# Kernel tuning notes

Hardware: AMD Instinct MI355X
Metric: run time of the kernel (lower is better)

Reference implementation:

```python
import jax, jax.numpy as jnp
import numpy as np

D_MODEL = 512
N_HEADS = 8
D_HEAD = D_MODEL // N_HEADS
D_FF = 2048
LN_EPS = 1e-5


def _layer_norm(x, g, b):
    mu = jnp.mean(x, axis=-1, keepdims=True)
    var = jnp.var(x, axis=-1, keepdims=True)
    return (x - mu) * jax.lax.rsqrt(var + LN_EPS) * g + b


def setup_inputs() -> dict:
    key = jax.random.key(0)
    ks = jax.random.split(key, 16)
    s_d = 1.0 / np.sqrt(D_MODEL)
    s_f = 1.0 / np.sqrt(D_FF)
    x = jax.random.normal(ks[0], (32, 512, D_MODEL), dtype=jnp.float32)
    # per-head Q/K/V linears stacked over heads: [H, D, dh] weights, [H, dh] biases
    Wq = jax.random.uniform(ks[1], (N_HEADS, D_MODEL, D_HEAD), jnp.float32, -s_d, s_d)
    bq = jax.random.uniform(ks[2], (N_HEADS, D_HEAD), jnp.float32, -s_d, s_d)
    Wk = jax.random.uniform(ks[3], (N_HEADS, D_MODEL, D_HEAD), jnp.float32, -s_d, s_d)
    bk = jax.random.uniform(ks[4], (N_HEADS, D_HEAD), jnp.float32, -s_d, s_d)
    Wv = jax.random.uniform(ks[5], (N_HEADS, D_MODEL, D_HEAD), jnp.float32, -s_d, s_d)
    bv = jax.random.uniform(ks[6], (N_HEADS, D_HEAD), jnp.float32, -s_d, s_d)
    Wo = jax.random.uniform(ks[7], (D_MODEL, D_MODEL), jnp.float32, -s_d, s_d)
    bo = jax.random.uniform(ks[8], (D_MODEL,), jnp.float32, -s_d, s_d)
    ln1_g = jnp.ones((D_MODEL,), jnp.float32)
    ln1_b = jnp.zeros((D_MODEL,), jnp.float32)
    W1 = jax.random.uniform(ks[9], (D_MODEL, D_FF), jnp.float32, -s_d, s_d)
    b1 = jax.random.uniform(ks[10], (D_FF,), jnp.float32, -s_d, s_d)
    W2 = jax.random.uniform(ks[11], (D_FF, D_MODEL), jnp.float32, -s_f, s_f)
    b2 = jax.random.uniform(ks[12], (D_MODEL,), jnp.float32, -s_f, s_f)
    ln2_g = jnp.ones((D_MODEL,), jnp.float32)
    ln2_b = jnp.zeros((D_MODEL,), jnp.float32)
    return dict(x=x, Wq=Wq, bq=bq, Wk=Wk, bk=bk, Wv=Wv, bv=bv, Wo=Wo, bo=bo,
                ln1_g=ln1_g, ln1_b=ln1_b, W1=W1, b1=b1, W2=W2, b2=b2,
                ln2_g=ln2_g, ln2_b=ln2_b)


def reference(x, Wq, bq, Wk, bk, Wv, bv, Wo, bo, ln1_g, ln1_b, W1, b1, W2, b2, ln2_g, ln2_b):
    B, T, D = x.shape
    # batched-heads Q/K/V: [B, H, T, dh]
    q = jnp.einsum('btd,hde->bhte', x, Wq) + bq[None, :, None, :]
    k = jnp.einsum('btd,hde->bhte', x, Wk) + bk[None, :, None, :]
    v = jnp.einsum('btd,hde->bhte', x, Wv) + bv[None, :, None, :]
    scale = D_HEAD ** -0.5
    scores = jnp.einsum('bhte,bhse->bhts', q, k) * scale  # [B,H,T,T]
    causal = jnp.tril(jnp.ones((T, T), dtype=bool))
    scores = jnp.where(causal[None, None], scores, -jnp.inf)
    w = jax.nn.softmax(scores, axis=-1)
    o = jnp.einsum('bhts,bhse->bhte', w, v)              # [B,H,T,dh]
    o = jnp.transpose(o, (0, 2, 1, 3)).reshape(B, T, D)   # concat heads
    attn = o @ Wo + bo
    out1 = x + _layer_norm(attn, ln1_g, ln1_b)            # post-LN on sublayer output (as in source)
    ff = jax.nn.relu(out1 @ W1 + b1) @ W2 + b2
    return out1 + _layer_norm(ff, ln2_g, ln2_b)
```

## Files before the change

kernel.cpp:

```cpp
#include <hip/hip_runtime.h>
#include <hip/hip_bf16.h>


#define D_MODEL 512
#define N_HEADS 8
#define D_HEAD 64
#define D_FF 2048
#define NROWS 16384

typedef __bf16 bf16x8 __attribute__((ext_vector_type(8)));
typedef float f32x4 __attribute__((ext_vector_type(4)));
typedef float f32x16 __attribute__((ext_vector_type(16)));

#define SWZ(x) ((x) ^ ((((x) >> 7) & 7) << 4))

static __device__ __forceinline__ ushort f2bf(float f) {
    union { float f; unsigned u; } v; v.f = f;
    unsigned r = v.u + 0x7fffu + ((v.u >> 16) & 1u);
    return (ushort)(r >> 16);
}
static __device__ __forceinline__ unsigned pack2(float lo, float hi) {
    return (unsigned)f2bf(lo) | ((unsigned)f2bf(hi) << 16);
}
static __device__ __forceinline__ void async16(const void* g, void* l) {
    __builtin_amdgcn_global_load_lds(
        (const __attribute__((address_space(1))) void*)g,
        (__attribute__((address_space(3))) void*)l, 16, 0, 0);
}

__global__ __launch_bounds__(256) void conv_bf_kernel(
    const float* __restrict__ src, ushort* __restrict__ dst, int n8)
{
    int i = blockIdx.x * 256 + threadIdx.x;
    if (i >= n8) return;
    const float4* s = (const float4*)src;
    float4 a = s[i * 2], b = s[i * 2 + 1];
    uint4 o;
    o.x = pack2(a.x, a.y); o.y = pack2(a.z, a.w);
    o.z = pack2(b.x, b.y); o.w = pack2(b.z, b.w);
    ((uint4*)dst)[i] = o;
}

static __device__ __forceinline__ void tile_transpose_body(
    const float* __restrict__ src, int srcldc, ushort* __restrict__ dst, int Rd,
    int r0, int c0)
{
    __shared__ float t[64][65];
    int tid = threadIdx.x;
    int lr = tid >> 4, lc4 = (tid & 15) * 4;
    #pragma unroll
    for (int i = 0; i < 4; ++i) {
        float4 v = *(const float4*)&src[(size_t)(r0 + lr + i * 16) * srcldc + c0 + lc4];
        t[lr + i * 16][lc4 + 0] = v.x;
        t[lr + i * 16][lc4 + 1] = v.y;
        t[lr + i * 16][lc4 + 2] = v.z;
        t[lr + i * 16][lc4 + 3] = v.w;
    }
    __syncthreads();
    int oc = tid >> 2, orr = (tid & 3) * 16;
    uint4 u0, u1;
    u0.x = pack2(t[orr + 0][oc],  t[orr + 1][oc]);
    u0.y = pack2(t[orr + 2][oc],  t[orr + 3][oc]);
    u0.z = pack2(t[orr + 4][oc],  t[orr + 5][oc]);
    u0.w = pack2(t[orr + 6][oc],  t[orr + 7][oc]);
    u1.x = pack2(t[orr + 8][oc],  t[orr + 9][oc]);
    u1.y = pack2(t[orr + 10][oc], t[orr + 11][oc]);
    u1.z = pack2(t[orr + 12][oc], t[orr + 13][oc]);
    u1.w = pack2(t[orr + 14][oc], t[orr + 15][oc]);
    ushort* d = dst + (size_t)(c0 + oc) * Rd + r0 + orr;
    *(uint4*)&d[0] = u0;
    *(uint4*)&d[8] = u1;
}

__global__ __launch_bounds__(256) void transpose_bf_kernel(
    const float* __restrict__ src, ushort* __restrict__ dst, int R, int C)
{
    tile_transpose_body(src, C, dst, R, blockIdx.y * 64, blockIdx.x * 64);
}

__global__ __launch_bounds__(256) void qkv_pack_kernel(
    const float* __restrict__ Wq, const float* __restrict__ Wk,
    const float* __restrict__ Wv, ushort* __restrict__ WpT)
{
    int z = blockIdx.z;
    int p = z >> 3, h = z & 7;
    const float* src = ((p == 0) ? Wq : (p == 1) ? Wk : Wv) + (size_t)h * D_MODEL * D_HEAD;
    ushort* dst = WpT + (size_t)(p * D_MODEL + h * D_HEAD) * D_MODEL;
    tile_transpose_body(src, D_HEAD, dst, D_MODEL, blockIdx.y * 64, 0);
}

__global__ __launch_bounds__(256) void pack_bias_kernel(
    const float* __restrict__ bq, const float* __restrict__ bk,
    const float* __restrict__ bv, float* __restrict__ bp)
{
    int idx = blockIdx.x * 256 + threadIdx.x;
    if (idx >= 3 * D_MODEL) return;
    int p = idx / D_MODEL;
    int h = (idx % D_MODEL) / D_HEAD;
    int e = idx % D_HEAD;
    const float* bb = (p == 0) ? bq : (p == 1) ? bk : bv;
    bp[idx] = bb[h * D_HEAD + e];
}

template<int OMODE, bool RELU>
__global__ __launch_bounds__(512, 1) void gemm_bf16_kernel(
    const ushort* __restrict__ A, const ushort* __restrict__ BT,
    const float* __restrict__ bias, void* __restrict__ Cout,
    ushort* __restrict__ Qg, ushort* __restrict__ Kg, ushort* __restrict__ Vt,
    int M, int N, int K, int nbx)
{
    extern __shared__ __align__(16) char smem[];

    const int tid = threadIdx.x;
    const int wid = tid >> 6, l = tid & 63;
    const int wr = wid >> 1, wc = wid & 1;

    const int total = gridDim.x;
    const int cpx = total >> 3;
    const int flat = blockIdx.x;
    const int swz = (flat & 7) * cpx + (flat >> 3);
    const int bx = swz % nbx, by = swz / nbx;
    const int m0 = by * 256, n0 = bx * 128;

    const int srow = tid >> 3;
    const int sbyte = (tid & 7) * 16;
    const int ssw = sbyte ^ ((srow & 7) << 4);

    #define STAGE(t)                                                          \
    {                                                                         \
        const int kk_ = (t) * 64;                                             \
        char* dst_ = smem + ((t) & 1) * 49152;                                \
        _Pragma("unroll")                                                     \
        for (int i = 0; i < 4; ++i)                                           \
            async16((const char*)(A + (size_t)(m0 + i * 64 + srow) * K + kk_) \
                        + ssw,                                                \
                    dst_ + i * 8192 + tid * 16);                              \
        _Pragma("unroll")                                                     \
        for (int i = 0; i < 2; ++i)                                           \
            async16((const char*)(BT + (size_t)(n0 + i * 64 + srow) * K + kk_)\
                        + ssw,                                                \
                    dst_ + 32768 + i * 8192 + tid * 16);                      \
    }

    const int fl = l & 31, fh = l >> 5;
    const int frsw = (fl & 7) << 4;

    f32x16 acc[2][2] = {};

    STAGE(0);
    const int T = K >> 6;
    for (int t = 0; t < T; ++t) {
        __builtin_amdgcn_s_barrier();
        if (t + 1 < T) {
            STAGE(t + 1);
            asm volatile("s_waitcnt vmcnt(6)" ::: "memory");
        } else {
            asm volatile("s_waitcnt vmcnt(0)" ::: "memory");
        }
        __builtin_amdgcn_sched_barrier(0);

        const char* bufA = smem + (t & 1) * 49152;
        const char* bufB = bufA + 32768;
        #pragma unroll
        for (int ks = 0; ks < 4; ++ks) {
            const int kb = ((ks * 32 + fh * 16) ^ frsw);
            bf16x8 af[2], bfv[2];
            #pragma unroll
            for (int mi = 0; mi < 2; ++mi)
                af[mi] = *(const bf16x8*)(bufA +
                    (wr * 64 + mi * 32 + fl) * 128 + kb);
            #pragma unroll
            for (int ni = 0; ni < 2; ++ni)
                bfv[ni] = *(const bf16x8*)(bufB +
                    (wc * 64 + ni * 32 + fl) * 128 + kb);
            #pragma unroll
            for (int mi = 0; mi < 2; ++mi)
                #pragma unroll
                for (int ni = 0; ni < 2; ++ni)
                    acc[mi][ni] = __builtin_amdgcn_mfma_f32_32x32x16_bf16(
                        af[mi], bfv[ni], acc[mi][ni], 0, 0, 0);
        }
    }

    #pragma unroll
    for (int ni = 0; ni < 2; ++ni) {
        const int c = n0 + wc * 64 + ni * 32 + fl;
        const float bvv = bias ? bias[c] : 0.f;
        #pragma unroll
        for (int mi = 0; mi < 2; ++mi) {
            const int rbase = m0 + wr * 64 + mi * 32 + (fh << 2);
            float vv[16];
            #pragma unroll
            for (int reg = 0; reg < 16; ++reg) {
                float v = acc[mi][ni][reg] + bvv;
                if (RELU) v = fmaxf(v, 0.f);
                vv[reg] = v;
            }
            if (OMODE == 0) {
                #pragma unroll
                for (int reg = 0; reg < 16; ++reg) {
                    int r = rbase + (reg & 3) + ((reg >> 2) << 3);
                    ((float*)Cout)[(size_t)r * N + c] = vv[reg];
                }
            } else if (OMODE == 1) {
                #pragma unroll
                for (int reg = 0; reg < 16; ++reg) {
                    int r = rbase + (reg & 3) + ((reg >> 2) << 3);
                    ((ushort*)Cout)[(size_t)r * N + c] = f2bf(vv[reg]);
                }
            } else {
                const int p = n0 >> 9;
                const int h = (c >> 6) & 7, e = c & 63;
                #pragma unroll
                for (int q = 0; q < 4; ++q) {
                    int r0 = rbase + (q << 3);
                    int b = r0 >> 9, t0 = r0 & 511;
                    size_t bh = (size_t)(b * 8 + h);
                    if (p == 2) {
                        uint2 pk;
                        pk.x = pack2(vv[q * 4 + 0], vv[q * 4 + 1]);
                        pk.y = pack2(vv[q * 4 + 2], vv[q * 4 + 3]);
                        *(uint2*)&Vt[bh * 32768 + (size_t)e * 512 + t0] = pk;
                    } else {
                        ushort* dst = (p == 0 ? Qg : Kg) + bh * 32768 +
                                      (size_t)t0 * 64 + e;
                        dst[0]   = f2bf(vv[q * 4 + 0]);
                        dst[64]  = f2bf(vv[q * 4 + 1]);
                        dst[128] = f2bf(vv[q * 4 + 2]);
                        dst[192] = f2bf(vv[q * 4 + 3]);
                    }
                }
            }
        }
    }
    #undef STAGE
}

__global__ __launch_bounds__(256) void attn_kernel(
    const ushort* __restrict__ Qg,
    const ushort* __restrict__ Kg,
    const ushort* __restrict__ Vt,
    ushort* __restrict__ O)
{
    __shared__ __align__(16) char QP[8192];
    __shared__ __align__(16) char KB[2][8192];
    __shared__ __align__(16) char VB[2][8192];

    const int bh = blockIdx.x, qb = blockIdx.y;
    const int tid = threadIdx.x;
    const int w = tid >> 6, l = tid & 63;

    const ushort* Qb = Qg + (size_t)bh * 32768;
    const ushort* Kb = Kg + (size_t)bh * 32768;
    const ushort* Vb = Vt + (size_t)bh * 32768;

    #pragma unroll
    for (int i = 0; i < 2; ++i) {
        int Xi = i * 4096 + tid * 16;
        int row = Xi >> 7;
        int sw = SWZ(Xi) & 127;
        async16((const char*)(Qb + (size_t)(qb * 64 + row) * 64) + sw, QP + Xi);
    }
    #define STAGEKV(kt, bb)                                                     \
        { _Pragma("unroll")                                                     \
          for (int i = 0; i < 2; ++i) {                                         \
              int Xi = i * 4096 + tid * 16;                                     \
              int row = Xi >> 7;                                                \
              int sw = SWZ(Xi) & 127;                                           \
              async16((const char*)(Kb + (size_t)((kt) * 64 + row) * 64) + sw,  \
                      KB[bb] + Xi);                                             \
              async16((const char*)(Vb + (size_t)row * 512 + (kt) * 64) + sw,   \
                      VB[bb] + Xi);                                             \
          } }
    STAGEKV(0, 0);
    __syncthreads();

    bf16x8 qf[2];
    {
        int qrow = w * 16 + (l & 15);
        #pragma unroll
        for (int ks = 0; ks < 2; ++ks) {
            int X = qrow * 128 + ks * 64 + (l >> 4) * 16;
            qf[ks] = *(const bf16x8*)(QP + SWZ(X));
        }
    }

    float mrow = -INFINITY, lrow = 0.f;
    f32x4 oacc[4] = {};

    for (int kt = 0; kt <= qb; ++kt) {
        int cur = kt & 1;
        if (kt < qb) STAGEKV(kt + 1, cur ^ 1);

        f32x4 sacc[4] = {};
        #pragma unroll
        for (int ks = 0; ks < 2; ++ks) {
            #pragma unroll
            for (int mi = 0; mi < 4; ++mi) {
                int X = (mi * 16 + (l & 15)) * 128 + ks * 64 + (l >> 4) * 16;
                bf16x8 kf = *(const bf16x8*)(KB[cur] + SWZ(X));
                sacc[mi] = __builtin_amdgcn_mfma_f32_16x16x32_bf16(
                    kf, qf[ks], sacc[mi], 0, 0, 0);
            }
        }

        float sv[16];
        float tmax = -INFINITY;
        const int qrow_t = w * 16 + (l & 15);
        #pragma unroll
        for (int mi = 0; mi < 4; ++mi)
            #pragma unroll
            for (int r = 0; r < 4; ++r) {
                float s = sacc[mi][r] * 0.125f;
                if (kt == qb) {
                    int key_l = mi * 16 + (l >> 4) * 4 + r;
                    if (key_l > qrow_t) s = -INFINITY;
                }
                sv[mi * 4 + r] = s;
                tmax = fmaxf(tmax, s);
            }
        tmax = fmaxf(tmax, __shfl_xor(tmax, 16));
        tmax = fmaxf(tmax, __shfl_xor(tmax, 32));
        float mnew = fmaxf(mrow, tmax);
        float corr = __expf(mrow - mnew);
        mrow = mnew;
        float psum = 0.f;
        #pragma unroll
        for (int i = 0; i < 16; ++i) { sv[i] = __expf(sv[i] - mnew); psum += sv[i]; }
        psum += __shfl_xor(psum, 16);
        psum += __shfl_xor(psum, 32);
        lrow = lrow * corr + psum;

        #pragma unroll
        for (int mi = 0; mi < 4; ++mi) {
            uint2 pk;
            pk.x = pack2(sv[mi * 4 + 0], sv[mi * 4 + 1]);
            pk.y = pack2(sv[mi * 4 + 2], sv[mi * 4 + 3]);
            int X = qrow_t * 128 + (mi * 16 + (l >> 4) * 4) * 2;
            *(uint2*)(QP + SWZ(X)) = pk;
        }

        #pragma unroll
        for (int r = 0; r < 4; ++r) {
            float cr = __shfl(corr, (l & 48) | ((l >> 4) * 4 + r));
            #pragma unroll
            for (int n = 0; n < 4; ++n) oacc[n][r] *= cr;
        }

        #pragma unroll
        for (int ks = 0; ks < 2; ++ks) {
            int Xa = qrow_t * 128 + ks * 64 + (l >> 4) * 16;
            bf16x8 pa = *(const bf16x8*)(QP + SWZ(Xa));
            #pragma unroll
            for (int n = 0; n < 4; ++n) {
                int Xb = (n * 16 + (l & 15)) * 128 + ks * 64 + (l >> 4) * 16;
                bf16x8 vb = *(const bf16x8*)(VB[cur] + SWZ(Xb));
                oacc[n] = __builtin_amdgcn_mfma_f32_16x16x32_bf16(
                    pa, vb, oacc[n], 0, 0, 0);
            }
        }
        __syncthreads();
    }

    float linv = 1.0f / lrow;
    const int b_ = bh >> 3, h_ = bh & 7;
    #pragma unroll
    for (int r = 0; r < 4; ++r) {
        float li = __shfl(linv, (l & 48) | ((l >> 4) * 4 + r));
        int trow = qb * 64 + w * 16 + (l >> 4) * 4 + r;
        size_t obase = ((size_t)b_ * 512 + trow) * 512 + h_ * 64 + (l & 15);
        #pragma unroll
        for (int n = 0; n < 4; ++n)
            O[obase + n * 16] = f2bf(oacc[n][r] * li);
    }
}

template<bool WBF>
__global__ __launch_bounds__(256) void ln_res_kernel(
    const float* __restrict__ v, const float* __restrict__ res,
    const float* __restrict__ g, const float* __restrict__ bb,
    float* __restrict__ out, ushort* __restrict__ out_bf)
{
    int row  = blockIdx.x * 4 + (threadIdx.x >> 6);
    int lane = threadIdx.x & 63;
    const float4* vp = (const float4*)(v + (size_t)row * D_MODEL);
    float4 a = vp[lane];
    float4 c = vp[lane + 64];
    float sum = a.x + a.y + a.z + a.w + c.x + c.y + c.z + c.w;
    float sq  = a.x*a.x + a.y*a.y + a.z*a.z + a.w*a.w
              + c.x*c.x + c.y*c.y + c.z*c.z + c.w*c.w;
    #pragma unroll
    for (int o = 1; o < 64; o <<= 1) {
        sum += __shfl_xor(sum, o);
        sq  += __shfl_xor(sq, o);
    }
    float mu   = sum * (1.f / 512.f);
    float var  = sq * (1.f / 512.f) - mu * mu;
    float rstd = rsqrtf(var + 1e-5f);

    const float4* rp = (const float4*)(res + (size_t)row * D_MODEL);
    const float4* gp = (const float4*)g;
    const float4* bp = (const float4*)bb;
    float4 r0 = rp[lane], r1 = rp[lane + 64];
    float4 g0 = gp[lane], g1 = gp[lane + 64];
    float4 b0 = bp[lane], b1 = bp[lane + 64];
    float4 o0, o1;
    o0.x = r0.x + (a.x - mu) * rstd * g0.x + b0.x;
    o0.y = r0.y + (a.y - mu) * rstd * g0.y + b0.y;
    o0.z = r0.z + (a.z - mu) * rstd * g0.z + b0.z;
    o0.w = r0.w + (a.w - mu) * rstd * g0.w + b0.w;
    o1.x = r1.x + (c.x - mu) * rstd * g1.x + b1.x;
    o1.y = r1.y + (c.y - mu) * rstd * g1.y + b1.y;
    o1.z = r1.z + (c.z - mu) * rstd * g1.z + b1.z;
    o1.w = r1.w + (c.w - mu) * rstd * g1.w + b1.w;
    float4* op = (float4*)(out + (size_t)row * D_MODEL);
    op[lane] = o0;
    op[lane + 64] = o1;
    if (WBF) {
        uint2 p0, p1;
        p0.x = pack2(o0.x, o0.y); p0.y = pack2(o0.z, o0.w);
        p1.x = pack2(o1.x, o1.y); p1.y = pack2(o1.z, o1.w);
        *(uint2*)&out_bf[(size_t)row * D_MODEL + lane * 4] = p0;
        *(uint2*)&out_bf[(size_t)row * D_MODEL + 256 + lane * 4] = p1;
    }
}

extern "C" void kernel_launch(void* const* d_in, const int* in_sizes, int n_in,
                              void* d_out, int out_size, void* d_ws, size_t ws_size,
                              hipStream_t stream)
{
    const float* x     = (const float*)d_in[0];
    const float* Wq    = (const float*)d_in[1];
    const float* bq    = (const float*)d_in[2];
    const float* Wk    = (const float*)d_in[3];
    const float* bk    = (const float*)d_in[4];
    const float* Wv    = (const float*)d_in[5];
    const float* bv    = (const float*)d_in[6];
    const float* Wo    = (const float*)d_in[7];
    const float* bo    = (const float*)d_in[8];
    const float* ln1_g = (const float*)d_in[9];
    const float* ln1_b = (const float*)d_in[10];
    const float* W1    = (const float*)d_in[11];
    const float* b1    = (const float*)d_in[12];
    const float* W2    = (const float*)d_in[13];
    const float* b2    = (const float*)d_in[14];
    const float* ln2_g = (const float*)d_in[15];
    const float* ln2_b = (const float*)d_in[16];

    float* ws = (float*)d_ws;
    ushort* Qg      = (ushort*)(ws);
    ushort* Kg      = (ushort*)(ws + 4194304);
    ushort* Vt      = (ushort*)(ws + 8388608);
    ushort* O_bf    = (ushort*)(ws + 12582912);
    float*  attnb   = ws + 16777216;
    float*  out1    = ws + 25165824;
    ushort* out1_bf = (ushort*)(ws + 33554432);
    ushort* x_bf    = (ushort*)(ws + 37748736);
    ushort* WpT     = (ushort*)(ws + 41943040);
    ushort* WoT     = (ushort*)(ws + 42336256);
    ushort* W1T     = (ushort*)(ws + 42467328);
    ushort* W2T     = (ushort*)(ws + 42991616);
    float*  bp      = ws + 43515904;
    ushort* ff1_bf  = (ushort*)ws;
    float*  ff2     = attnb;

    (void)hipFuncSetAttribute(
        reinterpret_cast<const void*>(&gemm_bf16_kernel<2, false>),
        hipFuncAttributeMaxDynamicSharedMemorySize, 98304);
    (void)hipFuncSetAttribute(
        reinterpret_cast<const void*>(&gemm_bf16_kernel<0, false>),
        hipFuncAttributeMaxDynamicSharedMemorySize, 98304);
    (void)hipFuncSetAttribute(
        reinterpret_cast<const void*>(&gemm_bf16_kernel<1, true>),
        hipFuncAttributeMaxDynamicSharedMemorySize, 98304);

    conv_bf_kernel<<<dim3(4096), 256, 0, stream>>>(x, x_bf, NROWS * D_MODEL / 8);
    qkv_pack_kernel<<<dim3(1, 8, 24), 256, 0, stream>>>(Wq, Wk, Wv, WpT);
    transpose_bf_kernel<<<dim3(8, 8), 256, 0, stream>>>(Wo, WoT, 512, 512);
    transpose_bf_kernel<<<dim3(32, 8), 256, 0, stream>>>(W1, W1T, 512, 2048);
    transpose_bf_kernel<<<dim3(8, 32), 256, 0, stream>>>(W2, W2T, 2048, 512);
    pack_bias_kernel<<<dim3(6), 256, 0, stream>>>(bq, bk, bv, bp);

    gemm_bf16_kernel<2, false><<<dim3(768), 512, 98304, stream>>>(
        x_bf, WpT, bp, nullptr, Qg, Kg, Vt, NROWS, 1536, 512, 12);

    attn_kernel<<<dim3(256, 8), 256, 0, stream>>>(Qg, Kg, Vt, O_bf);

    gemm_bf16_kernel<0, false><<<dim3(256), 512, 98304, stream>>>(
        O_bf, WoT, bo, attnb, nullptr, nullptr, nullptr, NROWS, 512, 512, 4);

    ln_res_kernel<true><<<dim3(NROWS / 4), 256, 0, stream>>>(
        attnb, x, ln1_g, ln1_b, out1, out1_bf);

    gemm_bf16_kernel<1, true><<<dim3(1024), 512, 98304, stream>>>(
        out1_bf, W1T, b1, ff1_bf, nullptr, nullptr, nullptr, NROWS, 2048, 512, 16);

    gemm_bf16_kernel<0, false><<<dim3(256), 512, 98304, stream>>>(
        ff1_bf, W2T, b2, ff2, nullptr, nullptr, nullptr, NROWS, 512, 2048, 4);

    ln_res_kernel<false><<<dim3(NROWS / 4), 256, 0, stream>>>(
        ff2, out1, ln2_g, ln2_b, (float*)d_out, nullptr);
}
```

Before: 224.0 us.

## Merge prep kernels, emit bf16 GEMM outputs for LN, restructure pipeline barriers

Six preprocessing launches (x conversion, weight transposes, bias pack) become a single prep kernel, cutting launch overhead. The Wo and W2 GEMMs now write bf16 instead of fp32, and the layer-norm kernels read bf16, halving that intermediate traffic. The GEMM main loop now issues the next stage's loads before computing and waits for all loads plus a barrier afterwards, in place of a partial vmcnt wait. Rounding the pre-LayerNorm activations to bf16 lowers accuracy.

```diff
diff --git a/kernel.cpp b/kernel.cpp
--- a/kernel.cpp
+++ b/kernel.cpp
@@ -22,23 +22,14 @@
 static __device__ __forceinline__ unsigned pack2(float lo, float hi) {
     return (unsigned)f2bf(lo) | ((unsigned)f2bf(hi) << 16);
 }
+static __device__ __forceinline__ float bf2f(ushort u) {
+    union { unsigned u; float f; } v; v.u = (unsigned)u << 16;
+    return v.f;
+}
 static __device__ __forceinline__ void async16(const void* g, void* l) {
     __builtin_amdgcn_global_load_lds(
         (const __attribute__((address_space(1))) void*)g,
         (__attribute__((address_space(3))) void*)l, 16, 0, 0);
-}
-
-__global__ __launch_bounds__(256) void conv_bf_kernel(
-    const float* __restrict__ src, ushort* __restrict__ dst, int n8)
-{
-    int i = blockIdx.x * 256 + threadIdx.x;
-    if (i >= n8) return;
-    const float4* s = (const float4*)src;
-    float4 a = s[i * 2], b = s[i * 2 + 1];
-    uint4 o;
-    o.x = pack2(a.x, a.y); o.y = pack2(a.z, a.w);
-    o.z = pack2(b.x, b.y); o.w = pack2(b.z, b.w);
-    ((uint4*)dst)[i] = o;
 }
 
 static __device__ __forceinline__ void tile_transpose_body(
@@ -72,34 +63,53 @@
     *(uint4*)&d[8] = u1;
 }
 
-__global__ __launch_bounds__(256) void transpose_bf_kernel(
-    const float* __restrict__ src, ushort* __restrict__ dst, int R, int C)
-{
-    tile_transpose_body(src, C, dst, R, blockIdx.y * 64, blockIdx.x * 64);
-}
-
-__global__ __launch_bounds__(256) void qkv_pack_kernel(
+__global__ __launch_bounds__(256) void prep_kernel(
+    const float* __restrict__ x, ushort* __restrict__ x_bf,
     const float* __restrict__ Wq, const float* __restrict__ Wk,
-    const float* __restrict__ Wv, ushort* __restrict__ WpT)
-{
-    int z = blockIdx.z;
-    int p = z >> 3, h = z & 7;
-    const float* src = ((p == 0) ? Wq : (p == 1) ? Wk : Wv) + (size_t)h * D_MODEL * D_HEAD;
-    ushort* dst = WpT + (size_t)(p * D_MODEL + h * D_HEAD) * D_MODEL;
-    tile_transpose_body(src, D_HEAD, dst, D_MODEL, blockIdx.y * 64, 0);
-}
-
-__global__ __launch_bounds__(256) void pack_bias_kernel(
+    const float* __restrict__ Wv, ushort* __restrict__ WpT,
+    const float* __restrict__ Wo, ushort* __restrict__ WoT,
+    const float* __restrict__ W1, ushort* __restrict__ W1T,
+    const float* __restrict__ W2, ushort* __restrict__ W2T,
     const float* __restrict__ bq, const float* __restrict__ bk,
     const float* __restrict__ bv, float* __restrict__ bp)
 {
-    int idx = blockIdx.x * 256 + threadIdx.x;
-    if (idx >= 3 * D_MODEL) return;
-    int p = idx / D_MODEL;
-    int h = (idx % D_MODEL) / D_HEAD;
-    int e = idx % D_HEAD;
-    const float* bb = (p == 0) ? bq : (p == 1) ? bk : bv;
-    bp[idx] = bb[h * D_HEAD + e];
+    const int blk = blockIdx.x;
+    const int tid = threadIdx.x;
+    if (blk < 4096) {
+        int i = blk * 256 + tid;
+        const float4* s = (const float4*)x;
+        float4 a = s[i * 2], b = s[i * 2 + 1];
+        uint4 o;
+        o.x = pack2(a.x, a.y); o.y = pack2(a.z, a.w);
+        o.z = pack2(b.x, b.y); o.w = pack2(b.z, b.w);
+        ((uint4*)x_bf)[i] = o;
+    } else if (blk < 4288) {
+        int idx = blk - 4096;
+        int z = idx >> 3, y = idx & 7;
+        int p = z >> 3, h = z & 7;
+        const float* src = ((p == 0) ? Wq : (p == 1) ? Wk : Wv) +
+                           (size_t)h * D_MODEL * D_HEAD;
+        ushort* dst = WpT + (size_t)(p * D_MODEL + h * D_HEAD) * D_MODEL;
+        tile_transpose_body(src, D_HEAD, dst, D_MODEL, y * 64, 0);
+    } else if (blk < 4352) {
+        int idx = blk - 4288;
+        tile_transpose_body(Wo, 512, WoT, 512, (idx >> 3) * 64, (idx & 7) * 64);
+    } else if (blk < 4608) {
+        int idx = blk - 4352;
+        tile_transpose_body(W1, 2048, W1T, 512, (idx >> 5) * 64, (idx & 31) * 64);
+    } else if (blk < 4864) {
+        int idx = blk - 4608;
+        tile_transpose_body(W2, 512, W2T, 2048, (idx >> 3) * 64, (idx & 7) * 64);
+    } else {
+        int gid = (blk - 4864) * 256 + tid;
+        if (gid < 3 * D_MODEL) {
+            int p = gid / D_MODEL;
+            int h = (gid % D_MODEL) / D_HEAD;
+            int e = gid % D_HEAD;
+            const float* bb = (p == 0) ? bq : (p == 1) ? bk : bv;
+            bp[gid] = bb[h * D_HEAD + e];
+        }
+    }
 }
 
 template<int OMODE, bool RELU>
@@ -115,8 +125,7 @@
     const int wid = tid >> 6, l = tid & 63;
     const int wr = wid >> 1, wc = wid & 1;
 
-    const int total = gridDim.x;
-    const int cpx = total >> 3;
+    const int cpx = gridDim.x >> 3;
     const int flat = blockIdx.x;
     const int swz = (flat & 7) * cpx + (flat >> 3);
     const int bx = swz % nbx, by = swz / nbx;
@@ -147,17 +156,14 @@
 
     f32x16 acc[2][2] = {};
 
+    const int T = K >> 6;
     STAGE(0);
-    const int T = K >> 6;
+    asm volatile("s_waitcnt vmcnt(0)" ::: "memory");
+    __builtin_amdgcn_s_barrier();
+    __builtin_amdgcn_sched_barrier(0);
+
     for (int t = 0; t < T; ++t) {
-        __builtin_amdgcn_s_barrier();
-        if (t + 1 < T) {
-            STAGE(t + 1);
-            asm volatile("s_waitcnt vmcnt(6)" ::: "memory");
-        } else {
-            asm volatile("s_waitcnt vmcnt(0)" ::: "memory");
-        }
-        __builtin_amdgcn_sched_barrier(0);
+        if (t + 1 < T) STAGE(t + 1);
 
         const char* bufA = smem + (t & 1) * 49152;
         const char* bufB = bufA + 32768;
@@ -180,7 +186,14 @@
                     acc[mi][ni] = __builtin_amdgcn_mfma_f32_32x32x16_bf16(
                         af[mi], bfv[ni], acc[mi][ni], 0, 0, 0);
         }
-    }
+
+        if (t + 1 < T) {
+            asm volatile("s_waitcnt vmcnt(0)" ::: "memory");
+            __builtin_amdgcn_s_barrier();
+            __builtin_amdgcn_sched_barrier(0);
+        }
+    }
+    #undef STAGE
 
     #pragma unroll
     for (int ni = 0; ni < 2; ++ni) {
@@ -196,13 +209,7 @@
                 if (RELU) v = fmaxf(v, 0.f);
                 vv[reg] = v;
             }
-            if (OMODE == 0) {
-                #pragma unroll
-                for (int reg = 0; reg < 16; ++reg) {
-                    int r = rbase + (reg & 3) + ((reg >> 2) << 3);
-                    ((float*)Cout)[(size_t)r * N + c] = vv[reg];
-                }
-            } else if (OMODE == 1) {
+            if (OMODE == 1) {
                 #pragma unroll
                 for (int reg = 0; reg < 16; ++reg) {
                     int r = rbase + (reg & 3) + ((reg >> 2) << 3);
@@ -233,7 +240,6 @@
             }
         }
     }
-    #undef STAGE
 }
 
 __global__ __launch_bounds__(256) void attn_kernel(
@@ -377,18 +383,24 @@
 
 template<bool WBF>
 __global__ __launch_bounds__(256) void ln_res_kernel(
-    const float* __restrict__ v, const float* __restrict__ res,
+    const ushort* __restrict__ v, const float* __restrict__ res,
     const float* __restrict__ g, const float* __restrict__ bb,
     float* __restrict__ out, ushort* __restrict__ out_bf)
 {
     int row  = blockIdx.x * 4 + (threadIdx.x >> 6);
     int lane = threadIdx.x & 63;
-    const float4* vp = (const float4*)(v + (size_t)row * D_MODEL);
-    float4 a = vp[lane];
-    float4 c = vp[lane + 64];
-    float sum = a.x + a.y + a.z + a.w + c.x + c.y + c.z + c.w;
-    float sq  = a.x*a.x + a.y*a.y + a.z*a.z + a.w*a.w
-              + c.x*c.x + c.y*c.y + c.z*c.z + c.w*c.w;
+    const int c0 = lane * 8;
+
+    uint4 vb = *(const uint4*)&v[(size_t)row * D_MODEL + c0];
+    float f[8];
+    f[0] = bf2f((ushort)(vb.x & 0xffff)); f[1] = bf2f((ushort)(vb.x >> 16));
+    f[2] = bf2f((ushort)(vb.y & 0xffff)); f[3] = bf2f((ushort)(vb.y >> 16));
+    f[4] = bf2f((ushort)(vb.z & 0xffff)); f[5] = bf2f((ushort)(vb.z >> 16));
+    f[6] = bf2f((ushort)(vb.w & 0xffff)); f[7] = bf2f((ushort)(vb.w >> 16));
+
+    float sum = 0.f, sq = 0.f;
+    #pragma unroll
+    for (int i = 0; i < 8; ++i) { sum += f[i]; sq += f[i] * f[i]; }
     #pragma unroll
     for (int o = 1; o < 64; o <<= 1) {
         sum += __shfl_xor(sum, o);
@@ -398,30 +410,29 @@
     float var  = sq * (1.f / 512.f) - mu * mu;
     float rstd = rsqrtf(var + 1e-5f);
 
-    const float4* rp = (const float4*)(res + (size_t)row * D_MODEL);
-    const float4* gp = (const float4*)g;
-    const float4* bp = (const float4*)bb;
-    float4 r0 = rp[lane], r1 = rp[lane + 64];
-    float4 g0 = gp[lane], g1 = gp[lane + 64];
-    float4 b0 = bp[lane], b1 = bp[lane + 64];
-    float4 o0, o1;
-    o0.x = r0.x + (a.x - mu) * rstd * g0.x + b0.x;
-    o0.y = r0.y + (a.y - mu) * rstd * g0.y + b0.y;
-    o0.z = r0.z + (a.z - mu) * rstd * g0.z + b0.z;
-    o0.w = r0.w + (a.w - mu) * rstd * g0.w + b0.w;
-    o1.x = r1.x + (c.x - mu) * rstd * g1.x + b1.x;
-    o1.y = r1.y + (c.y - mu) * rstd * g1.y + b1.y;
-    o1.z = r1.z + (c.z - mu) * rstd * g1.z + b1.z;
-    o1.w = r1.w + (c.w - mu) * rstd * g1.w + b1.w;
-    float4* op = (float4*)(out + (size_t)row * D_MODEL);
-    op[lane] = o0;
-    op[lane + 64] = o1;
+    float4 r0 = *(const float4*)&res[(size_t)row * D_MODEL + c0];
+    float4 r1 = *(const float4*)&res[(size_t)row * D_MODEL + c0 + 4];
+    float4 g0 = *(const float4*)&g[c0],  g1 = *(const float4*)&g[c0 + 4];
+    float4 b0 = *(const float4*)&bb[c0], b1 = *(const float4*)&bb[c0 + 4];
+
+    float o8[8];
+    o8[0] = r0.x + (f[0] - mu) * rstd * g0.x + b0.x;
+    o8[1] = r0.y + (f[1] - mu) * rstd * g0.y + b0.y;
+    o8[2] = r0.z + (f[2] - mu) * rstd * g0.z + b0.z;
+    o8[3] = r0.w + (f[3] - mu) * rstd * g0.w + b0.w;
+    o8[4] = r1.x + (f[4] - mu) * rstd * g1.x + b1.x;
+    o8[5] = r1.y + (f[5] - mu) * rstd * g1.y + b1.y;
+    o8[6] = r1.z + (f[6] - mu) * rstd * g1.z + b1.z;
+    o8[7] = r1.w + (f[7] - mu) * rstd * g1.w + b1.w;
+
+    float4* op = (float4*)&out[(size_t)row * D_MODEL + c0];
+    op[0] = make_float4(o8[0], o8[1], o8[2], o8[3]);
+    op[1] = make_float4(o8[4], o8[5], o8[6], o8[7]);
     if (WBF) {
-        uint2 p0, p1;
-        p0.x = pack2(o0.x, o0.y); p0.y = pack2(o0.z, o0.w);
-        p1.x = pack2(o1.x, o1.y); p1.y = pack2(o1.z, o1.w);
-        *(uint2*)&out_bf[(size_t)row * D_MODEL + lane * 4] = p0;
-        *(uint2*)&out_bf[(size_t)row * D_MODEL + 256 + lane * 4] = p1;
+        uint4 pk;
+        pk.x = pack2(o8[0], o8[1]); pk.y = pack2(o8[2], o8[3]);
+        pk.z = pack2(o8[4], o8[5]); pk.w = pack2(o8[6], o8[7]);
+        *(uint4*)&out_bf[(size_t)row * D_MODEL + c0] = pk;
     }
 }
 
@@ -452,52 +463,48 @@
     ushort* Kg      = (ushort*)(ws + 4194304);
     ushort* Vt      = (ushort*)(ws + 8388608);
     ushort* O_bf    = (ushort*)(ws + 12582912);
-    float*  attnb   = ws + 16777216;
-    float*  out1    = ws + 25165824;
-    ushort* out1_bf = (ushort*)(ws + 33554432);
-    ushort* x_bf    = (ushort*)(ws + 37748736);
+    ushort* attn_bf = (ushort*)(ws + 16777216);
+    float*  out1    = ws + 20971520;
+    ushort* out1_bf = (ushort*)(ws + 29360128);
+    ushort* x_bf    = (ushort*)(ws + 33554432);
+    ushort* ff2_bf  = (ushort*)(ws + 37748736);
     ushort* WpT     = (ushort*)(ws + 41943040);
     ushort* WoT     = (ushort*)(ws + 42336256);
     ushort* W1T     = (ushort*)(ws + 42467328);
     ushort* W2T     = (ushort*)(ws + 42991616);
     float*  bp      = ws + 43515904;
     ushort* ff1_bf  = (ushort*)ws;
-    float*  ff2     = attnb;
 
     (void)hipFuncSetAttribute(
         reinterpret_cast<const void*>(&gemm_bf16_kernel<2, false>),
         hipFuncAttributeMaxDynamicSharedMemorySize, 98304);
     (void)hipFuncSetAttribute(
-        reinterpret_cast<const void*>(&gemm_bf16_kernel<0, false>),
+        reinterpret_cast<const void*>(&gemm_bf16_kernel<1, false>),
         hipFuncAttributeMaxDynamicSharedMemorySize, 98304);
     (void)hipFuncSetAttribute(
         reinterpret_cast<const void*>(&gemm_bf16_kernel<1, true>),
         hipFuncAttributeMaxDynamicSharedMemorySize, 98304);
 
-    conv_bf_kernel<<<dim3(4096), 256, 0, stream>>>(x, x_bf, NROWS * D_MODEL / 8);
-    qkv_pack_kernel<<<dim3(1, 8, 24), 256, 0, stream>>>(Wq, Wk, Wv, WpT);
-    transpose_bf_kernel<<<dim3(8, 8), 256, 0, stream>>>(Wo, WoT, 512, 512);
-    transpose_bf_kernel<<<dim3(32, 8), 256, 0, stream>>>(W1, W1T, 512, 2048);
-    transpose_bf_kernel<<<dim3(8, 32), 256, 0, stream>>>(W2, W2T, 2048, 512);
-    pack_bias_kernel<<<dim3(6), 256, 0, stream>>>(bq, bk, bv, bp);
+    prep_kernel<<<dim3(4870), 256, 0, stream>>>(
+        x, x_bf, Wq, Wk, Wv, WpT, Wo, WoT, W1, W1T, W2, W2T, bq, bk, bv, bp);
 
     gemm_bf16_kernel<2, false><<<dim3(768), 512, 98304, stream>>>(
         x_bf, WpT, bp, nullptr, Qg, Kg, Vt, NROWS, 1536, 512, 12);
 
     attn_kernel<<<dim3(256, 8), 256, 0, stream>>>(Qg, Kg, Vt, O_bf);
 
-    gemm_bf16_kernel<0, false><<<dim3(256), 512, 98304, stream>>>(
-        O_bf, WoT, bo, attnb, nullptr, nullptr, nullptr, NROWS, 512, 512, 4);
+    gemm_bf16_kernel<1, false><<<dim3(256), 512, 98304, stream>>>(
+        O_bf, WoT, bo, attn_bf, nullptr, nullptr, nullptr, NROWS, 512, 512, 4);
 
     ln_res_kernel<true><<<dim3(NROWS / 4), 256, 0, stream>>>(
-        attnb, x, ln1_g, ln1_b, out1, out1_bf);
+        attn_bf, x, ln1_g, ln1_b, out1, out1_bf);
 
     gemm_bf16_kernel<1, true><<<dim3(1024), 512, 98304, stream>>>(
         out1_bf, W1T, b1, ff1_bf, nullptr, nullptr, nullptr, NROWS, 2048, 512, 16);
 
-    gemm_bf16_kernel<0, false><<<dim3(256), 512, 98304, stream>>>(
-        ff1_bf, W2T, b2, ff2, nullptr, nullptr, nullptr, NROWS, 512, 2048, 4);
+    gemm_bf16_kernel<1, false><<<dim3(256), 512, 98304, stream>>>(
+        ff1_bf, W2T, b2, ff2_bf, nullptr, nullptr, nullptr, NROWS, 512, 2048, 4);
 
     ln_res_kernel<false><<<dim3(NROWS / 4), 256, 0, stream>>>(
-        ff2, out1, ln2_g, ln2_b, (float*)d_out, nullptr);
-}
+        ff2_bf, out1, ln2_g, ln2_b, (float*)d_out, nullptr);
+}
```

After: 211.7 us, median of 2. -5.5%, faster.
